# Performance work log

Hardware: AMD Instinct MI355X
Metric: run time of the kernel (lower is better)

The kernel has to match this reference:

```python
import jax, jax.numpy as jnp
import numpy as np

N_NODES = 100000
N_EDGES = 3200000
IN_DIM = 11
HID = 32


def setup_inputs() -> dict:
    key = jax.random.key(0)
    ks = jax.random.split(key, 12)
    inp = {
        "x": jax.random.normal(ks[0], (N_NODES, IN_DIM), dtype=jnp.float32),
        "edge_index": jax.random.randint(ks[1], (2, N_EDGES), 0, N_NODES, dtype=jnp.int32),
        "batch": jnp.zeros((N_NODES,), dtype=jnp.int32),
        # GCNConv layer 1 (11 -> 32)
        "W1": jax.random.normal(ks[2], (IN_DIM, HID), dtype=jnp.float32) / np.sqrt(IN_DIM),
        "b1": jnp.zeros((HID,), dtype=jnp.float32),
        # GCNConv layer 2 (32 -> 32)
        "W2": jax.random.normal(ks[3], (HID, HID), dtype=jnp.float32) / np.sqrt(HID),
        "b2": jnp.zeros((HID,), dtype=jnp.float32),
        # output MLP: 32 -> 16 -> 1
        "Wo1": jax.random.normal(ks[4], (HID, HID // 2), dtype=jnp.float32) / np.sqrt(HID),
        "bo1": jnp.zeros((HID // 2,), dtype=jnp.float32),
        "Wo2": jax.random.normal(ks[5], (HID // 2, 1), dtype=jnp.float32) / np.sqrt(HID // 2),
        "bo2": jnp.zeros((1,), dtype=jnp.float32),
    }
    return inp


def _gcn_norm(edge_index, n_nodes):
    # Add self-loops and compute symmetric normalization (PyG GCNConv default).
    loops = jnp.arange(n_nodes, dtype=edge_index.dtype)
    src = jnp.concatenate([edge_index[0], loops])
    dst = jnp.concatenate([edge_index[1], loops])
    ones = jnp.ones_like(dst, dtype=jnp.float32)
    deg = jax.ops.segment_sum(ones, dst, num_segments=n_nodes)  # degree of A+I on target side
    dinv = jax.lax.rsqrt(deg)  # deg >= 1 thanks to self-loops
    norm = dinv[src] * dinv[dst]  # [E+N]
    return src, dst, norm


def _gcn_conv(x, W, b, src, dst, norm, n_nodes):
    xw = x @ W                                   # transform first (small dim)
    msg = norm[:, None] * xw[src]                # gather + scale  [E+N, H]
    agg = jax.ops.segment_sum(msg, dst, num_segments=n_nodes)  # scatter-add
    return agg + b


def reference(x, edge_index, batch, W1, b1, W2, b2, Wo1, bo1, Wo2, bo2):
    n = x.shape[0]
    src, dst, norm = _gcn_norm(edge_index, n)
    h = jax.nn.relu(_gcn_conv(x, W1, b1, src, dst, norm, n))
    # F.dropout(training=self.training) is identity in eval mode
    h = jax.nn.relu(_gcn_conv(h, W2, b2, src, dst, norm, n))
    h = jax.nn.elu(h @ Wo1 + bo1)
    out = h @ Wo2 + bo2
    return out.squeeze(-1)  # [N]
```

## Files before the change

### kernel.cpp

```cpp
#include <hip/hip_runtime.h>
#include <hip/hip_fp16.h>
#include <math.h>

#define N_NODES 100000
#define N_EDGES 3200000
#define IN_DIM 11
#define HID 32
#define HID2 16
#define SCHUNK 100352
#define BINSHIFT 8
#define BINSZ 256
#define NB 391
#define CHUNK 4096
#define NCH 782

__global__ __launch_bounds__(256) void k_hist(const int* __restrict__ ei,
                                              int* __restrict__ cnthist) {
    __shared__ int h[NB];
    int t = threadIdx.x;
    for (int i = t; i < NB; i += 256) h[i] = 0;
    __syncthreads();
    int b0 = blockIdx.x * CHUNK;
    int n = N_EDGES - b0; if (n > CHUNK) n = CHUNK;
    for (int e = t * 4; e < n; e += 1024) {
        int4 d4 = *(const int4*)(ei + N_EDGES + b0 + e);
        atomicAdd(&h[d4.x >> BINSHIFT], 1);
        atomicAdd(&h[d4.y >> BINSHIFT], 1);
        atomicAdd(&h[d4.z >> BINSHIFT], 1);
        atomicAdd(&h[d4.w >> BINSHIFT], 1);
    }
    __syncthreads();
    for (int i = t; i < NB; i += 256)
        cnthist[i * NCH + blockIdx.x] = h[i];
}

__global__ __launch_bounds__(256) void k_colscan(int* __restrict__ cnthist,
                                                 int* __restrict__ colsum) {
    __shared__ int tmp[256];
    int i = blockIdx.x;
    int t = threadIdx.x;
    int v[4];
    int s4 = 0;
#pragma unroll
    for (int u = 0; u < 4; ++u) {
        int idx = t * 4 + u;
        v[u] = (idx < NCH) ? cnthist[i * NCH + idx] : 0;
        s4 += v[u];
    }
    tmp[t] = s4;
    __syncthreads();
    for (int off = 1; off < 256; off <<= 1) {
        int u = (t >= off) ? tmp[t - off] : 0;
        __syncthreads();
        tmp[t] += u;
        __syncthreads();
    }
    int base = tmp[t] - s4;
#pragma unroll
    for (int u = 0; u < 4; ++u) {
        int idx = t * 4 + u;
        if (idx < NCH) cnthist[i * NCH + idx] = base;
        base += v[u];
    }
    if (t == 255) colsum[i] = tmp[255];
}

__global__ __launch_bounds__(512) void k_scanbins(const int* __restrict__ colsum,
                                                  int* __restrict__ binbase) {
    __shared__ int tmp[512];
    int t = threadIdx.x;
    int v = (t < NB) ? colsum[t] : 0;
    tmp[t] = v;
    __syncthreads();
    for (int off = 1; off < 512; off <<= 1) {
        int u = (t >= off) ? tmp[t - off] : 0;
        __syncthreads();
        tmp[t] += u;
        __syncthreads();
    }
    if (t < NB) binbase[t] = tmp[t] - v;
    if (t == 0) binbase[NB] = N_EDGES;
}

__global__ __launch_bounds__(512) void k_binscatter(const int* __restrict__ ei,
                                                    const int* __restrict__ binbase,
                                                    const int* __restrict__ cnthist,
                                                    unsigned* __restrict__ binbuf) {
    __shared__ unsigned short sbin[CHUNK];
    __shared__ unsigned char  sdl[CHUNK];
    __shared__ unsigned       srecS[CHUNK];
    __shared__ unsigned short sbinS[CHUNK];
    __shared__ int h[NB], rl[NB], gb[NB];
    __shared__ int tmp[512];
    int t = threadIdx.x;
    int b0 = blockIdx.x * CHUNK;
    int n = N_EDGES - b0; if (n > CHUNK) n = CHUNK;
    for (int i = t; i < NB; i += 512) h[i] = 0;
    __syncthreads();
    for (int e = t; e < n; e += 512) {
        int d = ei[N_EDGES + b0 + e];
        int b = d >> BINSHIFT;
        sbin[e] = (unsigned short)b;
        sdl[e]  = (unsigned char)(d & (BINSZ - 1));
        atomicAdd(&h[b], 1);
    }
    __syncthreads();
    int c = (t < NB) ? h[t] : 0;
    tmp[t] = c;
    __syncthreads();
    for (int off = 1; off < 512; off <<= 1) {
        int u = (t >= off) ? tmp[t - off] : 0;
        __syncthreads();
        tmp[t] += u;
        __syncthreads();
    }
    if (t < NB) {
        rl[t] = tmp[t] - c;
        gb[t] = binbase[t] + cnthist[t * NCH + blockIdx.x];
        h[t] = 0;
    }
    __syncthreads();
    for (int e = t; e < n; e += 512) {
        int s = ei[b0 + e];
        int b = sbin[e];
        int p = rl[b] + atomicAdd(&h[b], 1);
        srecS[p] = (unsigned)s | ((unsigned)sdl[e] << 17);
        sbinS[p] = (unsigned short)b;
    }
    __syncthreads();
    for (int p = t; p < n; p += 512) {
        int b = sbinS[p];
        binbuf[gb[b] + (p - rl[b])] = srecS[p];
    }
}

__global__ __launch_bounds__(256) void k_binfill(const unsigned* __restrict__ binbuf,
                                                 const int* __restrict__ binbase,
                                                 int* __restrict__ rowstart,
                                                 float* __restrict__ dinv,
                                                 int* __restrict__ csr_src) {
    int bb = blockIdx.x;
    int b = bb >> 1;
    int half = bb & 1;
    int t = threadIdx.x;
    __shared__ int cnt[BINSZ], rloc[BINSZ], cur[BINSZ], tmp[BINSZ];
    int ebeg = binbase[b], eend = binbase[b + 1];
    cnt[t] = 0;
    __syncthreads();
    for (int e = ebeg + t; e < eend; e += 256)
        atomicAdd(&cnt[binbuf[e] >> 17], 1);
    __syncthreads();
    int c = cnt[t];
    tmp[t] = c;
    __syncthreads();
    for (int off = 1; off < 256; off <<= 1) {
        int u = (t >= off) ? tmp[t - off] : 0;
        __syncthreads();
        tmp[t] += u;
        __syncthreads();
    }
    rloc[t] = tmp[t] - c;
    cur[t] = 0;
    int node = b * BINSZ + t;
    if ((t >> 7) == half && node < N_NODES) {
        rowstart[node] = ebeg + rloc[t];
        dinv[node] = rsqrtf((float)c + 1.0f);
    }
    if (bb == 0 && t == 0) rowstart[N_NODES] = N_EDGES;
    __syncthreads();
    for (int e = ebeg + t; e < eend; e += 256) {
        unsigned vv = binbuf[e];
        int dl = vv >> 17;
        if ((dl >> 7) == half) {
            int p = ebeg + rloc[dl] + atomicAdd(&cur[dl], 1);
            csr_src[p] = (int)(vv & 0x1FFFFu);
        }
    }
}

__global__ void k_xw1(const float* __restrict__ x, const float* __restrict__ W1,
                      const float* __restrict__ dinv, __half* __restrict__ xwh) {
    int t = blockIdx.x * blockDim.x + threadIdx.x;
    int node = t >> 5;
    int j = t & 31;
    __shared__ float sW[IN_DIM * HID];
    __shared__ float sx[8 * IN_DIM];
    for (int i = threadIdx.x; i < IN_DIM * HID; i += 256) sW[i] = W1[i];
    int base = blockIdx.x * 8;
    if (threadIdx.x < 8 * IN_DIM) sx[threadIdx.x] = x[base * IN_DIM + threadIdx.x];
    __syncthreads();
    int ln = node - base;
    float acc = 0.0f;
#pragma unroll
    for (int k = 0; k < IN_DIM; ++k)
        acc += sx[ln * IN_DIM + k] * sW[k * HID + j];
    xwh[t] = __float2half(dinv[node] * acc);
}

__device__ __forceinline__ void accum8(float* __restrict__ acc, const uint4 v) {
    float2 f0 = __half22float2(*(const __half2*)&v.x);
    float2 f1 = __half22float2(*(const __half2*)&v.y);
    float2 f2 = __half22float2(*(const __half2*)&v.z);
    float2 f3 = __half22float2(*(const __half2*)&v.w);
    acc[0] += f0.x; acc[1] += f0.y;
    acc[2] += f1.x; acc[3] += f1.y;
    acc[4] += f2.x; acc[5] += f2.y;
    acc[6] += f3.x; acc[7] += f3.y;
}

__device__ __forceinline__ void edge_accum8(int beg, int end, int q, int oj,
                                            const int* __restrict__ csr_src,
                                            const __half* __restrict__ xwh,
                                            float* __restrict__ acc) {
#pragma unroll
    for (int k = 0; k < 8; ++k) acc[k] = 0.0f;
    int e = beg;
    for (; e + 32 <= end; e += 32) {
        int s0 = csr_src[e + q];
        int s1 = csr_src[e + 8 + q];
        int s2 = csr_src[e + 16 + q];
        int s3 = csr_src[e + 24 + q];
        uint4 v0 = *(const uint4*)(xwh + ((s0 << 5) | oj));
        uint4 v1 = *(const uint4*)(xwh + ((s1 << 5) | oj));
        uint4 v2 = *(const uint4*)(xwh + ((s2 << 5) | oj));
        uint4 v3 = *(const uint4*)(xwh + ((s3 << 5) | oj));
        accum8(acc, v0); accum8(acc, v1); accum8(acc, v2); accum8(acc, v3);
    }
    if (e + 16 <= end) {
        int s0 = csr_src[e + q];
        int s1 = csr_src[e + 8 + q];
        uint4 v0 = *(const uint4*)(xwh + ((s0 << 5) | oj));
        uint4 v1 = *(const uint4*)(xwh + ((s1 << 5) | oj));
        accum8(acc, v0); accum8(acc, v1);
        e += 16;
    }
    if (e + 8 <= end) {
        int s0 = csr_src[e + q];
        uint4 v0 = *(const uint4*)(xwh + ((s0 << 5) | oj));
        accum8(acc, v0);
        e += 8;
    }
    if (e + q < end) {
        int s0 = csr_src[e + q];
        uint4 v0 = *(const uint4*)(xwh + ((s0 << 5) | oj));
        accum8(acc, v0);
    }
#pragma unroll
    for (int m = 4; m <= 16; m <<= 1) {
#pragma unroll
        for (int k = 0; k < 8; ++k) acc[k] += __shfl_xor(acc[k], m);
    }
}

__global__ __launch_bounds__(256) void k_gather_xw2(const int* __restrict__ rowstart,
                                                    const float* __restrict__ dinv,
                                                    const int* __restrict__ csr_src,
                                                    const __half* __restrict__ xwh1,
                                                    const float* __restrict__ b1,
                                                    const float* __restrict__ W2,
                                                    __half* __restrict__ xwh2) {
    __shared__ float sW2[HID * HID];
    __shared__ float sA[8][33];
    __shared__ float sH[8][33];
    for (int i = threadIdx.x; i < HID * HID; i += 256) sW2[i] = W2[i];

    int ln = threadIdx.x >> 5;
    int node = blockIdx.x * 8 + ln;
    int l = threadIdx.x & 31;
    int q = l >> 2;
    int oj = (l & 3) << 3;

    float acc[8];
    edge_accum8(rowstart[node], rowstart[node + 1], q, oj, csr_src, xwh1, acc);
    if (q == 0) {
#pragma unroll
        for (int k = 0; k < 8; ++k) sA[ln][oj + k] = acc[k];
    }
    __syncthreads();

    int j = l;
    float dd = dinv[node];
    float hv = dd * (sA[ln][j] + __half2float(xwh1[node * HID + j])) + b1[j];
    sH[ln][j] = hv > 0.0f ? hv : 0.0f;
    __syncthreads();

    float a2 = 0.0f;
#pragma unroll
    for (int k = 0; k < HID; ++k) a2 += sH[ln][k] * sW2[k * HID + j];
    xwh2[node * HID + j] = __float2half(dd * a2);
}

__global__ __launch_bounds__(256) void k_gather_mlp(const int* __restrict__ rowstart,
                                                    const float* __restrict__ dinv,
                                                    const int* __restrict__ csr_src,
                                                    const __half* __restrict__ xwh,
                                                    const float* __restrict__ b2,
                                                    const float* __restrict__ Wo1,
                                                    const float* __restrict__ bo1,
                                                    const float* __restrict__ Wo2,
                                                    const float* __restrict__ bo2,
                                                    float* __restrict__ out) {
    __shared__ float sW1[HID * HID2];
    __shared__ float sb1[HID2];
    __shared__ float sW2v[HID2];
    __shared__ float sb2[HID];
    __shared__ float sA[8][33];
    __shared__ float sH[8][33];
    for (int i = threadIdx.x; i < HID * HID2; i += 256) sW1[i] = Wo1[i];
    if (threadIdx.x < HID2) {
        sb1[threadIdx.x] = bo1[threadIdx.x];
        sW2v[threadIdx.x] = Wo2[threadIdx.x];
    }
    if (threadIdx.x < HID) sb2[threadIdx.x] = b2[threadIdx.x];

    int ln = threadIdx.x >> 5;
    int node = blockIdx.x * 8 + ln;
    int l = threadIdx.x & 31;
    int q = l >> 2;
    int oj = (l & 3) << 3;

    float acc[8];
    edge_accum8(rowstart[node], rowstart[node + 1], q, oj, csr_src, xwh, acc);
    if (q == 0) {
#pragma unroll
        for (int k = 0; k < 8; ++k) sA[ln][oj + k] = acc[k];
    }
    __syncthreads();

    int j = l;
    float dd = dinv[node];
    float hv = dd * (sA[ln][j] + __half2float(xwh[node * HID + j])) + sb2[j];
    sH[ln][j] = hv > 0.0f ? hv : 0.0f;
    __syncthreads();

    float val = 0.0f;
    if (j < HID2) {
        float a = sb1[j];
#pragma unroll
        for (int k = 0; k < HID; ++k) a += sH[ln][k] * sW1[k * HID2 + j];
        a = a > 0.0f ? a : (expf(a) - 1.0f);
        val = a * sW2v[j];
    }
#pragma unroll
    for (int d = 16; d >= 1; d >>= 1) val += __shfl_down(val, d, 32);
    if (j == 0) out[node] = val + bo2[0];
}

extern "C" void kernel_launch(void* const* d_in, const int* in_sizes, int n_in,
                              void* d_out, int out_size, void* d_ws, size_t ws_size,
                              hipStream_t stream) {
    const float* x   = (const float*)d_in[0];
    const int*   ei  = (const int*)d_in[1];
    const float* W1  = (const float*)d_in[3];
    const float* b1  = (const float*)d_in[4];
    const float* W2  = (const float*)d_in[5];
    const float* b2  = (const float*)d_in[6];
    const float* Wo1 = (const float*)d_in[7];
    const float* bo1 = (const float*)d_in[8];
    const float* Wo2 = (const float*)d_in[9];
    const float* bo2 = (const float*)d_in[10];
    float* out = (float*)d_out;

    int*      colsum   = (int*)d_ws;
    int*      binbase  = colsum + 512;
    int*      rowstart = binbase + 512;
    float*    dinv     = (float*)(rowstart + SCHUNK);
    int*      csr_src  = (int*)(dinv + SCHUNK);
    unsigned* binbuf   = (unsigned*)(csr_src + N_EDGES);
    __half*   XWH1     = (__half*)(binbuf + N_EDGES);
    __half*   XWH2     = XWH1 + (size_t)N_NODES * HID;
    int*      cnthist  = csr_src;

    const int BT = 256;
    int gNH  = (N_NODES * HID + BT - 1) / BT;
    int gG   = N_NODES / 8;

    k_hist      <<<NCH, BT, 0, stream>>>(ei, cnthist);
    k_colscan   <<<NB, BT, 0, stream>>>(cnthist, colsum);
    k_scanbins  <<<1, 512, 0, stream>>>(colsum, binbase);
    k_binscatter<<<NCH, 512, 0, stream>>>(ei, binbase, cnthist, binbuf);
    k_binfill   <<<2 * NB, BT, 0, stream>>>(binbuf, binbase, rowstart, dinv, csr_src);

    k_xw1<<<gNH, BT, 0, stream>>>(x, W1, dinv, XWH1);
    k_gather_xw2<<<gG, BT, 0, stream>>>(rowstart, dinv, csr_src, XWH1, b1, W2, XWH2);

    k_gather_mlp<<<gG, BT, 0, stream>>>(rowstart, dinv, csr_src, XWH2,
                                        b2, Wo1, bo1, Wo2, bo2, out);
}
```

Baseline: 252.6 us.

## Fuse CSR build and first transform into one cooperative persistent kernel

Merges the histogram, column scan, bin scan, bin scatter, bin fill and first feature transform into a single cooperative kernel, with grid.sync between phases. The edge chunk stays in shared memory from the histogram pass through the scatter, so the destination array is read once instead of twice. This is meant to remove five kernel launches and one global read of the edge list. In exchange it adds five grid-wide barriers, and every block must be resident at once, which limits occupancy and tiles the later phases over fewer blocks.

```diff
diff --git a/kernel.cpp b/kernel.cpp
--- a/kernel.cpp
+++ b/kernel.cpp
@@ -1,6 +1,9 @@
 #include <hip/hip_runtime.h>
+#include <hip/hip_cooperative_groups.h>
 #include <hip/hip_fp16.h>
 #include <math.h>
+
+namespace cg = cooperative_groups;
 
 #define N_NODES 100000
 #define N_EDGES 3200000
@@ -11,91 +14,42 @@
 #define BINSHIFT 8
 #define BINSZ 256
 #define NB 391
-#define CHUNK 4096
-#define NCH 782
-
-__global__ __launch_bounds__(256) void k_hist(const int* __restrict__ ei,
-                                              int* __restrict__ cnthist) {
-    __shared__ int h[NB];
-    int t = threadIdx.x;
-    for (int i = t; i < NB; i += 256) h[i] = 0;
-    __syncthreads();
-    int b0 = blockIdx.x * CHUNK;
+#define CHUNK 4224
+#define NCH 758
+
+#define OFF_SREC  0
+#define OFF_SBINS 16896
+#define OFF_SBIN  25344
+#define OFF_SDL   33792
+#define OFF_H     38016
+#define OFF_RL    40064
+#define OFF_TMP   42112
+#define POOLSZ    44160
+
+__global__ __launch_bounds__(512, 6) void k_build(
+    const int* __restrict__ ei, int* __restrict__ cnthist,
+    int* __restrict__ colsum, int* __restrict__ binbase,
+    unsigned* __restrict__ binbuf, int* __restrict__ rowstart,
+    float* __restrict__ dinv, int* __restrict__ csr_src,
+    const float* __restrict__ x, const float* __restrict__ W1,
+    __half* __restrict__ xwh1)
+{
+    cg::grid_group grid = cg::this_grid();
+    __shared__ __align__(16) unsigned char pool[POOLSZ];
+    unsigned*       srecS = (unsigned*)(pool + OFF_SREC);
+    unsigned short* sbinS = (unsigned short*)(pool + OFF_SBINS);
+    unsigned short* sbin  = (unsigned short*)(pool + OFF_SBIN);
+    unsigned char*  sdl   = (unsigned char*)(pool + OFF_SDL);
+    int* h   = (int*)(pool + OFF_H);
+    int* rl  = (int*)(pool + OFF_RL);
+    int* tmp = (int*)(pool + OFF_TMP);
+
+    const int blk = blockIdx.x;
+    const int t = threadIdx.x;
+    const int b0 = blk * CHUNK;
     int n = N_EDGES - b0; if (n > CHUNK) n = CHUNK;
-    for (int e = t * 4; e < n; e += 1024) {
-        int4 d4 = *(const int4*)(ei + N_EDGES + b0 + e);
-        atomicAdd(&h[d4.x >> BINSHIFT], 1);
-        atomicAdd(&h[d4.y >> BINSHIFT], 1);
-        atomicAdd(&h[d4.z >> BINSHIFT], 1);
-        atomicAdd(&h[d4.w >> BINSHIFT], 1);
-    }
-    __syncthreads();
-    for (int i = t; i < NB; i += 256)
-        cnthist[i * NCH + blockIdx.x] = h[i];
-}
-
-__global__ __launch_bounds__(256) void k_colscan(int* __restrict__ cnthist,
-                                                 int* __restrict__ colsum) {
-    __shared__ int tmp[256];
-    int i = blockIdx.x;
-    int t = threadIdx.x;
-    int v[4];
-    int s4 = 0;
-#pragma unroll
-    for (int u = 0; u < 4; ++u) {
-        int idx = t * 4 + u;
-        v[u] = (idx < NCH) ? cnthist[i * NCH + idx] : 0;
-        s4 += v[u];
-    }
-    tmp[t] = s4;
-    __syncthreads();
-    for (int off = 1; off < 256; off <<= 1) {
-        int u = (t >= off) ? tmp[t - off] : 0;
-        __syncthreads();
-        tmp[t] += u;
-        __syncthreads();
-    }
-    int base = tmp[t] - s4;
-#pragma unroll
-    for (int u = 0; u < 4; ++u) {
-        int idx = t * 4 + u;
-        if (idx < NCH) cnthist[i * NCH + idx] = base;
-        base += v[u];
-    }
-    if (t == 255) colsum[i] = tmp[255];
-}
-
-__global__ __launch_bounds__(512) void k_scanbins(const int* __restrict__ colsum,
-                                                  int* __restrict__ binbase) {
-    __shared__ int tmp[512];
-    int t = threadIdx.x;
-    int v = (t < NB) ? colsum[t] : 0;
-    tmp[t] = v;
-    __syncthreads();
-    for (int off = 1; off < 512; off <<= 1) {
-        int u = (t >= off) ? tmp[t - off] : 0;
-        __syncthreads();
-        tmp[t] += u;
-        __syncthreads();
-    }
-    if (t < NB) binbase[t] = tmp[t] - v;
-    if (t == 0) binbase[NB] = N_EDGES;
-}
-
-__global__ __launch_bounds__(512) void k_binscatter(const int* __restrict__ ei,
-                                                    const int* __restrict__ binbase,
-                                                    const int* __restrict__ cnthist,
-                                                    unsigned* __restrict__ binbuf) {
-    __shared__ unsigned short sbin[CHUNK];
-    __shared__ unsigned char  sdl[CHUNK];
-    __shared__ unsigned       srecS[CHUNK];
-    __shared__ unsigned short sbinS[CHUNK];
-    __shared__ int h[NB], rl[NB], gb[NB];
-    __shared__ int tmp[512];
-    int t = threadIdx.x;
-    int b0 = blockIdx.x * CHUNK;
-    int n = N_EDGES - b0; if (n > CHUNK) n = CHUNK;
-    for (int i = t; i < NB; i += 512) h[i] = 0;
+
+    h[t] = 0;
     __syncthreads();
     for (int e = t; e < n; e += 512) {
         int d = ei[N_EDGES + b0 + e];
@@ -105,7 +59,7 @@
         atomicAdd(&h[b], 1);
     }
     __syncthreads();
-    int c = (t < NB) ? h[t] : 0;
+    int c = h[t];
     tmp[t] = c;
     __syncthreads();
     for (int off = 1; off < 512; off <<= 1) {
@@ -114,11 +68,9 @@
         tmp[t] += u;
         __syncthreads();
     }
-    if (t < NB) {
-        rl[t] = tmp[t] - c;
-        gb[t] = binbase[t] + cnthist[t * NCH + blockIdx.x];
-        h[t] = 0;
-    }
+    rl[t] = tmp[t] - c;
+    h[t] = 0;
+    if (t < NB) cnthist[t * NCH + blk] = c;
     __syncthreads();
     for (int e = t; e < n; e += 512) {
         int s = ei[b0 + e];
@@ -127,74 +79,111 @@
         srecS[p] = (unsigned)s | ((unsigned)sdl[e] << 17);
         sbinS[p] = (unsigned short)b;
     }
+    grid.sync();
+
+    if (blk < NB) {
+        int i0 = t * 2, i1 = t * 2 + 1;
+        int v0 = (i0 < NCH) ? cnthist[blk * NCH + i0] : 0;
+        int v1 = (i1 < NCH) ? cnthist[blk * NCH + i1] : 0;
+        int s2 = v0 + v1;
+        tmp[t] = s2;
+        __syncthreads();
+        for (int off = 1; off < 512; off <<= 1) {
+            int u = (t >= off) ? tmp[t - off] : 0;
+            __syncthreads();
+            tmp[t] += u;
+            __syncthreads();
+        }
+        int base = tmp[t] - s2;
+        if (i0 < NCH) cnthist[blk * NCH + i0] = base;
+        if (i1 < NCH) cnthist[blk * NCH + i1] = base + v0;
+        if (t == 511) colsum[blk] = tmp[511];
+    }
+    grid.sync();
+
+    if (blk == 0) {
+        int v = (t < NB) ? colsum[t] : 0;
+        tmp[t] = v;
+        __syncthreads();
+        for (int off = 1; off < 512; off <<= 1) {
+            int u = (t >= off) ? tmp[t - off] : 0;
+            __syncthreads();
+            tmp[t] += u;
+            __syncthreads();
+        }
+        if (t < NB) binbase[t] = tmp[t] - v;
+        if (t == 0) binbase[NB] = N_EDGES;
+    }
+    grid.sync();
+
+    if (t < NB) tmp[t] = binbase[t] + cnthist[t * NCH + blk];
     __syncthreads();
     for (int p = t; p < n; p += 512) {
         int b = sbinS[p];
-        binbuf[gb[b] + (p - rl[b])] = srecS[p];
-    }
-}
-
-__global__ __launch_bounds__(256) void k_binfill(const unsigned* __restrict__ binbuf,
-                                                 const int* __restrict__ binbase,
-                                                 int* __restrict__ rowstart,
-                                                 float* __restrict__ dinv,
-                                                 int* __restrict__ csr_src) {
-    int bb = blockIdx.x;
-    int b = bb >> 1;
-    int half = bb & 1;
-    int t = threadIdx.x;
-    __shared__ int cnt[BINSZ], rloc[BINSZ], cur[BINSZ], tmp[BINSZ];
-    int ebeg = binbase[b], eend = binbase[b + 1];
-    cnt[t] = 0;
-    __syncthreads();
-    for (int e = ebeg + t; e < eend; e += 256)
-        atomicAdd(&cnt[binbuf[e] >> 17], 1);
-    __syncthreads();
-    int c = cnt[t];
-    tmp[t] = c;
-    __syncthreads();
-    for (int off = 1; off < 256; off <<= 1) {
-        int u = (t >= off) ? tmp[t - off] : 0;
-        __syncthreads();
-        tmp[t] += u;
-        __syncthreads();
-    }
-    rloc[t] = tmp[t] - c;
-    cur[t] = 0;
-    int node = b * BINSZ + t;
-    if ((t >> 7) == half && node < N_NODES) {
-        rowstart[node] = ebeg + rloc[t];
-        dinv[node] = rsqrtf((float)c + 1.0f);
-    }
-    if (bb == 0 && t == 0) rowstart[N_NODES] = N_EDGES;
-    __syncthreads();
-    for (int e = ebeg + t; e < eend; e += 256) {
-        unsigned vv = binbuf[e];
-        int dl = vv >> 17;
-        if ((dl >> 7) == half) {
-            int p = ebeg + rloc[dl] + atomicAdd(&cur[dl], 1);
-            csr_src[p] = (int)(vv & 0x1FFFFu);
-        }
-    }
-}
-
-__global__ void k_xw1(const float* __restrict__ x, const float* __restrict__ W1,
-                      const float* __restrict__ dinv, __half* __restrict__ xwh) {
-    int t = blockIdx.x * blockDim.x + threadIdx.x;
-    int node = t >> 5;
-    int j = t & 31;
-    __shared__ float sW[IN_DIM * HID];
-    __shared__ float sx[8 * IN_DIM];
-    for (int i = threadIdx.x; i < IN_DIM * HID; i += 256) sW[i] = W1[i];
-    int base = blockIdx.x * 8;
-    if (threadIdx.x < 8 * IN_DIM) sx[threadIdx.x] = x[base * IN_DIM + threadIdx.x];
-    __syncthreads();
-    int ln = node - base;
-    float acc = 0.0f;
-#pragma unroll
-    for (int k = 0; k < IN_DIM; ++k)
-        acc += sx[ln * IN_DIM + k] * sW[k * HID + j];
-    xwh[t] = __float2half(dinv[node] * acc);
+        binbuf[tmp[b] + (p - rl[b])] = srecS[p];
+    }
+    grid.sync();
+
+    int* cnt  = (int*)(pool + OFF_SBIN);
+    int* rloc = (int*)(pool + OFF_SBIN + 1024);
+    int* cur  = (int*)(pool + OFF_SBIN + 2048);
+    int* tm2  = (int*)(pool + OFF_SBIN + 3072);
+    for (int task = blk; task < 2 * NB; task += NCH) {
+        int b = task >> 1, half = task & 1;
+        int ebeg = binbase[b], eend = binbase[b + 1];
+        if (t < BINSZ) cnt[t] = 0;
+        __syncthreads();
+        for (int e = ebeg + t; e < eend; e += 512)
+            atomicAdd(&cnt[binbuf[e] >> 17], 1);
+        __syncthreads();
+        int cc = (t < BINSZ) ? cnt[t] : 0;
+        if (t < BINSZ) tm2[t] = cc;
+        __syncthreads();
+        for (int off = 1; off < BINSZ; off <<= 1) {
+            int u = (t < BINSZ && t >= off) ? tm2[t - off] : 0;
+            __syncthreads();
+            if (t < BINSZ) tm2[t] += u;
+            __syncthreads();
+        }
+        if (t < BINSZ) {
+            rloc[t] = tm2[t] - cc;
+            cur[t] = 0;
+            int node = b * BINSZ + t;
+            if ((t >> 7) == half && node < N_NODES) {
+                rowstart[node] = ebeg + rloc[t];
+                dinv[node] = rsqrtf((float)cc + 1.0f);
+            }
+        }
+        __syncthreads();
+        for (int e = ebeg + t; e < eend; e += 512) {
+            unsigned vv = binbuf[e];
+            int dl = vv >> 17;
+            if ((dl >> 7) == half) {
+                int p = ebeg + rloc[dl] + atomicAdd(&cur[dl], 1);
+                csr_src[p] = (int)(vv & 0x1FFFFu);
+            }
+        }
+        __syncthreads();
+    }
+    if (blk == 0 && t == 0) rowstart[N_NODES] = N_EDGES;
+    grid.sync();
+
+    float* sW = (float*)(pool + OFF_SREC);
+    float* sx = (float*)(pool + OFF_SREC + 2048);
+    for (int i = t; i < IN_DIM * HID; i += 512) sW[i] = W1[i];
+    __syncthreads();
+    for (int task = blk; task < N_NODES / 16; task += NCH) {
+        if (t < 16 * IN_DIM) sx[t] = x[task * 16 * IN_DIM + t];
+        __syncthreads();
+        int ln = t >> 5, j = t & 31;
+        int node = task * 16 + ln;
+        float acc = 0.0f;
+#pragma unroll
+        for (int k = 0; k < IN_DIM; ++k)
+            acc += sx[ln * IN_DIM + k] * sW[k * HID + j];
+        xwh1[node * HID + j] = __float2half(dinv[node] * acc);
+        __syncthreads();
+    }
 }
 
 __device__ __forceinline__ void accum8(float* __restrict__ acc, const uint4 v) {
@@ -372,16 +361,14 @@
     int*      cnthist  = csr_src;
 
     const int BT = 256;
-    int gNH  = (N_NODES * HID + BT - 1) / BT;
-    int gG   = N_NODES / 8;
-
-    k_hist      <<<NCH, BT, 0, stream>>>(ei, cnthist);
-    k_colscan   <<<NB, BT, 0, stream>>>(cnthist, colsum);
-    k_scanbins  <<<1, 512, 0, stream>>>(colsum, binbase);
-    k_binscatter<<<NCH, 512, 0, stream>>>(ei, binbase, cnthist, binbuf);
-    k_binfill   <<<2 * NB, BT, 0, stream>>>(binbuf, binbase, rowstart, dinv, csr_src);
-
-    k_xw1<<<gNH, BT, 0, stream>>>(x, W1, dinv, XWH1);
+    int gG = N_NODES / 8;
+
+    void* kargs[] = { (void*)&ei, (void*)&cnthist, (void*)&colsum, (void*)&binbase,
+                      (void*)&binbuf, (void*)&rowstart, (void*)&dinv, (void*)&csr_src,
+                      (void*)&x, (void*)&W1, (void*)&XWH1 };
+    hipLaunchCooperativeKernel((const void*)k_build, dim3(NCH), dim3(512),
+                               kargs, 0, stream);
+
     k_gather_xw2<<<gG, BT, 0, stream>>>(rowstart, dinv, csr_src, XWH1, b1, W2, XWH2);
 
     k_gather_mlp<<<gG, BT, 0, stream>>>(rowstart, dinv, csr_src, XWH2,
```

Result: slower. 678.2 us (+168.5%).
